# Optimization experiments

Measured on AMD Instinct MI355X. Metric: run time of the kernel, lower is better.

The kernel has to match this reference:

```python
import jax, jax.numpy as jnp
import numpy as np

D_MODEL = 1024
N_HEAD = 16
D_HEAD = D_MODEL // N_HEAD
D_FF = 4096
B, S = 2, 2048
EPS = 1e-5


def setup_inputs() -> dict:
    key = jax.random.key(0)
    ks = jax.random.split(key, 16)
    sc = 1.0 / np.sqrt(D_MODEL)
    x = jax.random.normal(ks[0], (B, S, D_MODEL), dtype=jnp.float32)
    # causal mask: 1 where attention is disallowed (upper triangle)
    mask = jnp.triu(jnp.ones((S, S), dtype=jnp.int32), k=1)[None, None]
    p = {
        'x': x,
        'mask': mask,
        'wq': jax.random.normal(ks[1], (D_MODEL, D_MODEL), jnp.float32) * sc,
        'bq': jnp.zeros((D_MODEL,), jnp.float32),
        'wk': jax.random.normal(ks[2], (D_MODEL, D_MODEL), jnp.float32) * sc,
        'bk': jnp.zeros((D_MODEL,), jnp.float32),
        'wv': jax.random.normal(ks[3], (D_MODEL, D_MODEL), jnp.float32) * sc,
        'bv': jnp.zeros((D_MODEL,), jnp.float32),
        'wo': jax.random.normal(ks[4], (D_MODEL, D_MODEL), jnp.float32) * sc,
        'bo': jnp.zeros((D_MODEL,), jnp.float32),
        'w1': jax.random.normal(ks[5], (D_MODEL, D_FF), jnp.float32) * sc,
        'b1': jnp.zeros((D_FF,), jnp.float32),
        'w2': jax.random.normal(ks[6], (D_FF, D_MODEL), jnp.float32) * (1.0 / np.sqrt(D_FF)),
        'b2': jnp.zeros((D_MODEL,), jnp.float32),
        'g1': jnp.ones((D_MODEL,), jnp.float32),
        'beta1': jnp.zeros((D_MODEL,), jnp.float32),
        'g2': jnp.ones((D_MODEL,), jnp.float32),
        'beta2': jnp.zeros((D_MODEL,), jnp.float32),
    }
    return p


def _layer_norm(x, g, b):
    mu = jnp.mean(x, axis=-1, keepdims=True)
    var = jnp.mean(jnp.square(x - mu), axis=-1, keepdims=True)
    return (x - mu) * jax.lax.rsqrt(var + EPS) * g + b


def reference(x, mask, wq, bq, wk, bk, wv, bv, wo, bo, w1, b1, w2, b2, g1, beta1, g2, beta2):
    b, s, _ = x.shape
    # QKV projections -> [B, H, S, Dh]
    q = (x @ wq + bq).reshape(b, s, N_HEAD, D_HEAD).transpose(0, 2, 1, 3)
    k = (x @ wk + bk).reshape(b, s, N_HEAD, D_HEAD).transpose(0, 2, 1, 3)
    v = (x @ wv + bv).reshape(b, s, N_HEAD, D_HEAD).transpose(0, 2, 1, 3)
    scores = jnp.einsum('bhqd,bhkd->bhqk', q, k) / np.sqrt(D_HEAD)  # [B,H,S,S]
    scores = jnp.where(mask == 1, -jnp.inf, scores)
    attn = jax.nn.softmax(scores, axis=-1)
    out = jnp.einsum('bhqk,bhkd->bhqd', attn, v)
    out = out.transpose(0, 2, 1, 3).reshape(b, s, D_MODEL)
    attn_out = out @ wo + bo
    x1 = _layer_norm(x + attn_out, g1, beta1)
    ffn = jax.nn.relu(x1 @ w1 + b1) @ w2 + b2
    return _layer_norm(x1 + ffn, g2, beta2)
```

## Files before the change

kernel.cpp:

```cpp
#include <hip/hip_runtime.h>
#include <hip/hip_bf16.h>
#include <cstdint>

#define D_MODEL 1024
#define D_FF    4096
#define NHEAD   16
#define DHEAD   64
#define BATCH   2
#define SEQ     2048
#define BT      (BATCH*SEQ)
#define QKVLD   (3*D_MODEL)
#define LN_EPS  1e-5f

typedef __bf16 bf16_t;
typedef bf16_t bf16x8 __attribute__((ext_vector_type(8)));
typedef float  f32x4  __attribute__((ext_vector_type(4)));

__device__ __forceinline__ unsigned short f2b(float f){
  bf16_t h = (bf16_t)f;
  return __builtin_bit_cast(unsigned short, h);
}
__device__ __forceinline__ float b2f(unsigned short u){
  return __builtin_bit_cast(float, ((unsigned int)u)<<16);
}

__device__ __forceinline__ void gload16(const void* g, void* l){
  __builtin_amdgcn_global_load_lds(
      (const __attribute__((address_space(1))) unsigned int*)g,
      (__attribute__((address_space(3))) unsigned int*)l, 16, 0, 0);
}

__global__ __launch_bounds__(256) void cvt_f32_bf16(
    const float* __restrict__ in, unsigned short* __restrict__ out, int n){
  int i = (blockIdx.x*256 + threadIdx.x)*4;
  if (i < n){
    float4 v = *(const float4*)(in + i);
    ushort4 u; u.x=f2b(v.x); u.y=f2b(v.y); u.z=f2b(v.z); u.w=f2b(v.w);
    *(ushort4*)(out + i) = u;
  }
}

__global__ __launch_bounds__(256) void concat_bias(
    const float* __restrict__ bq, const float* __restrict__ bk,
    const float* __restrict__ bv, float* __restrict__ o){
  int i = blockIdx.x*256 + threadIdx.x;
  if (i < D_MODEL){ o[i]=bq[i]; o[D_MODEL+i]=bk[i]; o[2*D_MODEL+i]=bv[i]; }
}

__global__ __launch_bounds__(256) void transpose_cvt(
    const float* __restrict__ in, unsigned short* __restrict__ out, int R, int C){
  __shared__ float t[32][33];
  int c0 = blockIdx.x*32, r0 = blockIdx.y*32;
  int tx = threadIdx.x, ty = threadIdx.y;
  #pragma unroll
  for (int i=0;i<4;++i){ int r = ty + i*8; t[r][tx] = in[(size_t)(r0+r)*C + c0+tx]; }
  __syncthreads();
  #pragma unroll
  for (int i=0;i<4;++i){ int r = ty + i*8; out[(size_t)(c0+r)*R + r0+tx] = f2b(t[tx][r]); }
}

__global__ __launch_bounds__(256) void transpose_cvt4(
    const float* __restrict__ s0, const float* __restrict__ s1,
    const float* __restrict__ s2, const float* __restrict__ s3,
    unsigned short* __restrict__ d0, unsigned short* __restrict__ d1,
    unsigned short* __restrict__ d2, unsigned short* __restrict__ d3){
  __shared__ float t[32][33];
  int z = blockIdx.z;
  const float* in = (z==0)?s0:(z==1)?s1:(z==2)?s2:s3;
  unsigned short* out = (z==0)?d0:(z==1)?d1:(z==2)?d2:d3;
  int c0 = blockIdx.x*32, r0 = blockIdx.y*32;
  int tx = threadIdx.x, ty = threadIdx.y;
  #pragma unroll
  for (int i=0;i<4;++i){ int r = ty + i*8; t[r][tx] = in[(size_t)(r0+r)*D_MODEL + c0+tx]; }
  __syncthreads();
  #pragma unroll
  for (int i=0;i<4;++i){ int r = ty + i*8; out[(size_t)(c0+r)*D_MODEL + r0+tx] = f2b(t[tx][r]); }
}

template<int EPI>
__global__ __launch_bounds__(512,4) void gemm128(
    const unsigned short* __restrict__ A, const unsigned short* __restrict__ Bt,
    const float* __restrict__ bias, const float* __restrict__ resid,
    float* __restrict__ outF, unsigned short* __restrict__ outB,
    int M, int N, int K){
  __shared__ __attribute__((aligned(16))) unsigned short As[2][128*64];
  __shared__ __attribute__((aligned(16))) unsigned short Bs[2][128*64];
  int tid = threadIdx.x;
  int lane = tid & 63, wave = tid >> 6;
  int lr = lane & 15, lg = lane >> 4;
  int row0 = blockIdx.x*128, col0 = blockIdx.y*128;
  int wr = (wave>>2)*64, wc = (wave&3)*32;
  int x7 = lr & 7;

  int sr = tid >> 3;
  int sl = (tid & 7) ^ (sr & 7);
  auto STAGE = [&](int k0, int buf){
    #pragma unroll
    for (int it=0; it<2; ++it){
      int c = it*512 + tid;
      int r = it*64 + sr;
      gload16(A  + (size_t)(row0+r)*K + k0 + sl*8, &As[buf][c<<3]);
      gload16(Bt + (size_t)(col0+r)*K + k0 + sl*8, &Bs[buf][c<<3]);
    }
  };

  f32x4 acc[4][2] = {};
  int nk = K >> 6;
  int t0 = 0, t1 = nk;
  if (EPI==3){ int half = nk >> 1; t0 = blockIdx.z*half; t1 = t0 + half; }
  STAGE(t0<<6, 0);
  asm volatile("s_waitcnt vmcnt(0)" ::: "memory");
  __builtin_amdgcn_s_barrier();
  int cur = 0;
  for (int t=t0; t<t1; ++t){
    if (t+1 < t1) STAGE((t+1)<<6, cur^1);
    #pragma unroll
    for (int kk=0; kk<2; ++kk){
      int sk = ((kk*4 + lg) ^ x7) << 3;
      bf16x8 af[4], bfr[2];
      #pragma unroll
      for (int mi=0;mi<4;++mi) af[mi]  = *(const bf16x8*)&As[cur][(wr+mi*16+lr)*64 + sk];
      #pragma unroll
      for (int ni=0;ni<2;++ni) bfr[ni] = *(const bf16x8*)&Bs[cur][(wc+ni*16+lr)*64 + sk];
      #pragma unroll
      for (int mi=0;mi<4;++mi)
        #pragma unroll
        for (int ni=0;ni<2;++ni)
          acc[mi][ni] = __builtin_amdgcn_mfma_f32_16x16x32_bf16(af[mi], bfr[ni], acc[mi][ni], 0,0,0);
    }
    asm volatile("s_waitcnt vmcnt(0)" ::: "memory");
    __builtin_amdgcn_s_barrier();
    cur ^= 1;
  }
  unsigned short* outBP = (EPI==3) ? (outB + (size_t)blockIdx.z*((size_t)M*N)) : outB;
  #pragma unroll
  for (int mi=0;mi<4;++mi){
    int row = row0 + wr + mi*16 + (lg<<2);
    #pragma unroll
    for (int ni=0;ni<2;++ni){
      int col = col0 + wc + ni*16 + lr;
      float bs = (EPI==3) ? 0.f : bias[col];
      #pragma unroll
      for (int j=0;j<4;++j){
        size_t idx = (size_t)(row+j)*N + col;
        float v = acc[mi][ni][j] + bs;
        if (EPI==3){ outBP[idx] = f2b(v); }
        else if (EPI==2){ v = fmaxf(v, 0.f); outB[idx] = f2b(v); }
        else { outB[idx] = f2b(v); }
      }
    }
  }
}

template<int EPI>
__global__ __launch_bounds__(512,2) void gemm256(
    const unsigned short* __restrict__ A, const unsigned short* __restrict__ Bt,
    const float* __restrict__ bias, unsigned short* __restrict__ outB,
    unsigned short* __restrict__ outVt,
    int M, int N, int K){
  __shared__ __attribute__((aligned(16))) unsigned short As[2][2][128*64];
  __shared__ __attribute__((aligned(16))) unsigned short Bs[2][2][128*64];
  int tid = threadIdx.x;
  int lane = tid & 63, wave = tid >> 6;
  int lr = lane & 15, lg = lane >> 4;
  int wm = wave >> 2, wn = wave & 3;
  int row0 = blockIdx.x*256, col0 = blockIdx.y*256;
  int x7 = lr & 7;
  int sr = tid >> 3;
  int sl = (tid & 7) ^ (sr & 7);

  auto STAGE_A = [&](int t, int buf, int h){
    #pragma unroll
    for (int i=0;i<2;++i){
      int c = i*512 + tid;
      int r = i*64 + sr;
      gload16(A + (size_t)(row0 + h*128 + r)*K + t*64 + sl*8, &As[buf][h][c<<3]);
    }
  };
  auto STAGE_B = [&](int t, int buf, int h){
    #pragma unroll
    for (int i=0;i<2;++i){
      int c = i*512 + tid;
      int r = i*64 + sr;
      gload16(Bt + (size_t)(col0 + h*128 + r)*K + t*64 + sl*8, &Bs[buf][h][c<<3]);
    }
  };

  f32x4 acc[8][4] = {};
  int nk = K >> 6;
  STAGE_B(0,0,0); STAGE_B(0,0,1); STAGE_A(0,0,0); STAGE_A(0,0,1);
  asm volatile("s_waitcnt vmcnt(0)" ::: "memory");
  __builtin_amdgcn_s_barrier();
  int cur = 0;
  int bq = (wn&1)*64;
  for (int t=0; t<nk; ++t){
    bool pre = (t+1 < nk);
    const unsigned short* Ah = &As[cur][wm][0];
    const unsigned short* Bh = &Bs[cur][wn>>1][0];
    bf16x8 af[4][2], bfr[4][2];
    #pragma unroll
    for (int mi=0;mi<4;++mi)
      #pragma unroll
      for (int kk=0;kk<2;++kk)
        af[mi][kk] = *(const bf16x8*)&Ah[(mi*16+lr)*64 + (((kk*4+lg)^x7)<<3)];
    #pragma unroll
    for (int ni=0;ni<2;++ni)
      #pragma unroll
      for (int kk=0;kk<2;++kk)
        bfr[ni][kk] = *(const bf16x8*)&Bh[(bq+ni*16+lr)*64 + (((kk*4+lg)^x7)<<3)];
    if (pre){ STAGE_B(t+1, cur^1, 0);
              asm volatile("s_waitcnt vmcnt(2)" ::: "memory"); }
    else    { asm volatile("s_waitcnt vmcnt(0)" ::: "memory"); }
    __builtin_amdgcn_s_barrier();
    __builtin_amdgcn_s_setprio(1);
    #pragma unroll
    for (int mi=0;mi<4;++mi)
      #pragma unroll
      for (int ni=0;ni<2;++ni)
        #pragma unroll
        for (int kk=0;kk<2;++kk)
          acc[mi][ni] = __builtin_amdgcn_mfma_f32_16x16x32_bf16(af[mi][kk], bfr[ni][kk], acc[mi][ni], 0,0,0);
    __builtin_amdgcn_s_setprio(0);
    __builtin_amdgcn_s_barrier();
    #pragma unroll
    for (int ni=2;ni<4;++ni)
      #pragma unroll
      for (int kk=0;kk<2;++kk)
        bfr[ni][kk] = *(const bf16x8*)&Bh[(bq+ni*16+lr)*64 + (((kk*4+lg)^x7)<<3)];
    if (pre) STAGE_B(t+1, cur^1, 1);
    __builtin_amdgcn_s_barrier();
    __builtin_amdgcn_s_setprio(1);
    #pragma unroll
    for (int mi=0;mi<4;++mi)
      #pragma unroll
      for (int ni=2;ni<4;++ni)
        #pragma unroll
        for (int kk=0;kk<2;++kk)
          acc[mi][ni] = __builtin_amdgcn_mfma_f32_16x16x32_bf16(af[mi][kk], bfr[ni][kk], acc[mi][ni], 0,0,0);
    __builtin_amdgcn_s_setprio(0);
    __builtin_amdgcn_s_barrier();
    #pragma unroll
    for (int mi=0;mi<4;++mi)
      #pragma unroll
      for (int kk=0;kk<2;++kk)
        af[mi][kk] = *(const bf16x8*)&Ah[((mi+4)*16+lr)*64 + (((kk*4+lg)^x7)<<3)];
    if (pre) STAGE_A(t+1, cur^1, 0);
    __builtin_amdgcn_s_barrier();
    __builtin_amdgcn_s_setprio(1);
    #pragma unroll
    for (int mi=0;mi<4;++mi)
      #pragma unroll
      for (int ni=0;ni<2;++ni)
        #pragma unroll
        for (int kk=0;kk<2;++kk)
          acc[mi+4][ni] = __builtin_amdgcn_mfma_f32_16x16x32_bf16(af[mi][kk], bfr[ni][kk], acc[mi+4][ni], 0,0,0);
    __builtin_amdgcn_s_setprio(0);
    __builtin_amdgcn_s_barrier();
    if (pre) STAGE_A(t+1, cur^1, 1);
    __builtin_amdgcn_s_barrier();
    __builtin_amdgcn_s_setprio(1);
    #pragma unroll
    for (int mi=0;mi<4;++mi)
      #pragma unroll
      for (int ni=2;ni<4;++ni)
        #pragma unroll
        for (int kk=0;kk<2;++kk)
          acc[mi+4][ni] = __builtin_amdgcn_mfma_f32_16x16x32_bf16(af[mi][kk], bfr[ni][kk], acc[mi+4][ni], 0,0,0);
    __builtin_amdgcn_s_setprio(0);
    __builtin_amdgcn_s_barrier();
    cur ^= 1;
  }
  #pragma unroll
  for (int mi=0;mi<8;++mi){
    int row = row0 + wm*128 + mi*16 + (lg<<2);
    #pragma unroll
    for (int ni=0;ni<4;++ni){
      int col = col0 + wn*64 + ni*16 + lr;
      float bs = bias[col];
      ushort4 uu;
      #pragma unroll
      for (int j=0;j<4;++j){
        size_t idx = (size_t)(row+j)*N + col;
        float v = acc[mi][ni][j] + bs;
        if (EPI==2) v = fmaxf(v, 0.f);
        unsigned short us = f2b(v);
        outB[idx] = us;
        if (j==0) uu.x=us; else if (j==1) uu.y=us; else if (j==2) uu.z=us; else uu.w=us;
      }
      if (EPI==0 && outVt && col >= 2*D_MODEL){
        int vc = col - 2*D_MODEL;
        int bh = (row>>11)*NHEAD + (vc>>6);
        int d  = vc & 63;
        int s  = row & (SEQ-1);
        *(ushort4*)&outVt[((size_t)bh*DHEAD + d)*SEQ + s] = uu;
      }
    }
  }
}

__global__ __launch_bounds__(256,2) void attn_k(
    const unsigned short* __restrict__ QKV,
    const unsigned short* __restrict__ Vt, unsigned short* __restrict__ O){
  __shared__ __attribute__((aligned(16))) unsigned short Ks[2][128*64];
  __shared__ __attribute__((aligned(16))) unsigned short Vs[2][64*128];
  __shared__ __attribute__((aligned(16))) unsigned short Ps[4][16*128];
  int tid = threadIdx.x, lane = tid&63, wave = tid>>6;
  int lr = lane&15, lg = lane>>4;
  int bid = blockIdx.x;
  int L = (bid & 7)*64 + (bid >> 3);
  int qx = L & 15;
  int bh = L >> 4;
  int b = bh>>4, h = bh&15;
  const int NT = SEQ/64;
  const float SC2 = 0.18033688011112042f;

  #pragma unroll 1
  for (int half=0; half<2; ++half){
    int qt = half ? qx : (NT-1 - qx);
    int q0w = qt*64 + wave*16;

    const unsigned short* Qrow = QKV + (size_t)(b*SEQ + q0w + lr)*QKVLD + h*DHEAD;
    bf16x8 qf[2];
    qf[0] = *(const bf16x8*)(Qrow + lg*8);
    qf[1] = *(const bf16x8*)(Qrow + 32 + lg*8);

    f32x4 oacc[4] = {};
    float m2 = -1e30f, lsum = 0.f;

    auto STAGE = [&](int t, int buf){
      int kv0 = t*128;
      #pragma unroll
      for (int it=0; it<4; ++it){
        int c = it*256 + tid;
        int rk = c>>3, slk = (c&7) ^ (rk&7);
        gload16(QKV + (size_t)(b*SEQ + kv0 + rk)*QKVLD + D_MODEL + h*DHEAD + slk*8, &Ks[buf][c<<3]);
        int rv = c>>4, slv = (c&15) ^ (rv&15);
        gload16(Vt + ((size_t)bh*DHEAD + rv)*SEQ + kv0 + slv*8, &Vs[buf][c<<3]);
      }
    };

    int nkv = (qt + 2) >> 1;
    STAGE(0, 0);
    asm volatile("s_waitcnt vmcnt(0)" ::: "memory");
    __builtin_amdgcn_s_barrier();
    int cur = 0;
    for (int t=0; t<nkv; ++t){
      if (t+1 < nkv) STAGE(t+1, cur^1);

      int kv0 = t*128;
      f32x4 sacc[8] = {};
      #pragma unroll
      for (int kk=0;kk<2;++kk){
        #pragma unroll
        for (int ni=0;ni<8;++ni){
          int krow = ni*16 + lr;
          bf16x8 kf = *(const bf16x8*)&Ks[cur][krow*64 + (((kk*4+lg) ^ (krow&7))<<3)];
          sacc[ni] = __builtin_amdgcn_mfma_f32_16x16x32_bf16(kf, qf[kk], sacc[ni], 0,0,0);
        }
      }
      if (t == nkv-1){
        int qpos = q0w + lr;
        #pragma unroll
        for (int ni=0;ni<8;++ni){
          f32x4 v = sacc[ni];
          #pragma unroll
          for (int j=0;j<4;++j){
            int kpos = kv0 + ni*16 + lg*4 + j;
            float sv = v[j]*SC2;
            v[j] = (kpos > qpos) ? -1e30f : sv;
          }
          sacc[ni] = v;
        }
      } else {
        #pragma unroll
        for (int ni=0;ni<8;++ni) sacc[ni] *= SC2;
      }
      f32x4 vm = sacc[0];
      #pragma unroll
      for (int ni=1;ni<8;++ni)
        #pragma unroll
        for (int j=0;j<4;++j) vm[j] = fmaxf(vm[j], sacc[ni][j]);
      float rm = fmaxf(fmaxf(vm[0],vm[1]), fmaxf(vm[2],vm[3]));
      rm = fmaxf(rm, __shfl_xor(rm, 16));
      rm = fmaxf(rm, __shfl_xor(rm, 32));
      if (__all(rm <= m2)){
        f32x4 vs = {};
        #pragma unroll
        for (int ni=0;ni<8;++ni){
          f32x4 p;
          #pragma unroll
          for (int j=0;j<4;++j){ p[j] = exp2f(sacc[ni][j] - m2); vs[j] += p[j]; }
          sacc[ni] = p;
        }
        float rs = (vs[0]+vs[1]) + (vs[2]+vs[3]);
        rs += __shfl_xor(rs, 16);
        rs += __shfl_xor(rs, 32);
        lsum += rs;
      } else {
        float mnew = fmaxf(m2, rm);
        float corr = exp2f(m2 - mnew);
        m2 = mnew;
        f32x4 vs = {};
        #pragma unroll
        for (int ni=0;ni<8;++ni){
          f32x4 p;
          #pragma unroll
          for (int j=0;j<4;++j){ p[j] = exp2f(sacc[ni][j] - mnew); vs[j] += p[j]; }
          sacc[ni] = p;
        }
        float rs = (vs[0]+vs[1]) + (vs[2]+vs[3]);
        rs += __shfl_xor(rs, 16);
        rs += __shfl_xor(rs, 32);
        lsum = lsum*corr + rs;
        #pragma unroll
        for (int j=0;j<4;++j){
          float cj = __shfl(corr, lg*4 + j);
          #pragma unroll
          for (int nd=0; nd<4; ++nd) oacc[nd][j] *= cj;
        }
      }
      #pragma unroll
      for (int ni=0;ni<8;++ni){
        ushort4 u; u.x=f2b(sacc[ni][0]); u.y=f2b(sacc[ni][1]);
                   u.z=f2b(sacc[ni][2]); u.w=f2b(sacc[ni][3]);
        int ts = ni*2 + (lg>>1);
        int a = lr*128 + (((ts ^ lr))<<3) + ((lg&1)<<2);
        *(uint2*)&Ps[wave][a] = __builtin_bit_cast(uint2, u);
      }
      #pragma unroll
      for (int kk=0;kk<4;++kk){
        bf16x8 pa = *(const bf16x8*)&Ps[wave][lr*128 + (((kk*4+lg) ^ lr)<<3)];
        #pragma unroll
        for (int nd=0; nd<4; ++nd){
          int dr = nd*16 + lr;
          bf16x8 vf = *(const bf16x8*)&Vs[cur][dr*128 + (((kk*4+lg) ^ (dr&15))<<3)];
          oacc[nd] = __builtin_amdgcn_mfma_f32_16x16x32_bf16(pa, vf, oacc[nd], 0,0,0);
        }
      }
      asm volatile("s_waitcnt vmcnt(0)" ::: "memory");
      __builtin_amdgcn_s_barrier();
      cur ^= 1;
    }
    #pragma unroll
    for (int j=0;j<4;++j){
      float lj = __shfl(lsum, lg*4 + j);
      float inv = 1.f / lj;
      int token = b*SEQ + q0w + lg*4 + j;
      #pragma unroll
      for (int nd=0; nd<4; ++nd)
        O[(size_t)token*D_MODEL + h*DHEAD + nd*16 + lr] = f2b(oacc[nd][j]*inv);
    }
  }
}

template<int MODE>
__global__ __launch_bounds__(256) void ln_sum_k(
    const unsigned short* __restrict__ P,
    const float* __restrict__ bias,
    const float* __restrict__ resid,
    const float* __restrict__ g, const float* __restrict__ bta,
    float* __restrict__ outF, unsigned short* __restrict__ outB){
  int row = blockIdx.x, tid = threadIdx.x;
  const size_t MN = (size_t)BT*D_MODEL;
  ushort4 a0 = ((const ushort4*)(P + (size_t)row*D_MODEL))[tid];
  ushort4 a1 = ((const ushort4*)(P + MN + (size_t)row*D_MODEL))[tid];
  float4 rr = ((const float4*)(resid + (size_t)row*D_MODEL))[tid];
  float4 bb = ((const float4*)bias)[tid];
  float4 v;
  v.x = b2f(a0.x)+b2f(a1.x)+bb.x+rr.x; v.y = b2f(a0.y)+b2f(a1.y)+bb.y+rr.y;
  v.z = b2f(a0.z)+b2f(a1.z)+bb.z+rr.z; v.w = b2f(a0.w)+b2f(a1.w)+bb.w+rr.w;
  float s = v.x+v.y+v.z+v.w;
  float q = v.x*v.x+v.y*v.y+v.z*v.z+v.w*v.w;
  #pragma unroll
  for (int d=32; d; d>>=1){ s += __shfl_xor(s, d); q += __shfl_xor(q, d); }
  __shared__ float rs[4], rq[4];
  int wave = tid>>6;
  if ((tid&63)==0){ rs[wave]=s; rq[wave]=q; }
  __syncthreads();
  s = rs[0]+rs[1]+rs[2]+rs[3];
  q = rq[0]+rq[1]+rq[2]+rq[3];
  float mu  = s * (1.f/D_MODEL);
  float var = q * (1.f/D_MODEL) - mu*mu;
  float rstd = rsqrtf(var + LN_EPS);
  float4 gg = ((const float4*)g)[tid];
  float4 be = ((const float4*)bta)[tid];
  float o0 = (v.x-mu)*rstd*gg.x + be.x;
  float o1 = (v.y-mu)*rstd*gg.y + be.y;
  float o2 = (v.z-mu)*rstd*gg.z + be.z;
  float o3 = (v.w-mu)*rstd*gg.w + be.w;
  float4 o; o.x=o0; o.y=o1; o.z=o2; o.w=o3;
  ((float4*)(outF + (size_t)row*D_MODEL))[tid] = o;
  if (MODE==0){
    ushort4 u; u.x=f2b(o0); u.y=f2b(o1); u.z=f2b(o2); u.w=f2b(o3);
    ((ushort4*)(outB + (size_t)row*D_MODEL))[tid] = u;
  }
}

extern "C" void kernel_launch(void* const* d_in, const int* in_sizes, int n_in,
                              void* d_out, int out_size, void* d_ws, size_t ws_size,
                              hipStream_t stream){
  const float* x  = (const float*)d_in[0];
  const float* wq = (const float*)d_in[2];  const float* bq = (const float*)d_in[3];
  const float* wk = (const float*)d_in[4];  const float* bk = (const float*)d_in[5];
  const float* wv = (const float*)d_in[6];  const float* bv = (const float*)d_in[7];
  const float* wo = (const float*)d_in[8];  const float* bo = (const float*)d_in[9];
  const float* w1 = (const float*)d_in[10]; const float* b1 = (const float*)d_in[11];
  const float* w2 = (const float*)d_in[12]; const float* b2 = (const float*)d_in[13];
  const float* g1 = (const float*)d_in[14]; const float* be1= (const float*)d_in[15];
  const float* g2 = (const float*)d_in[16]; const float* be2= (const float*)d_in[17];

  char* w = (char*)d_ws;
  size_t off = 0;
  auto nxt = [&](size_t bytes)->void*{
    void* p = w + off; off = (off + bytes + 255) & ~(size_t)255; return p;
  };
  unsigned short* xb    = (unsigned short*)nxt((size_t)BT*D_MODEL*2);
  unsigned short* wqkvT = (unsigned short*)nxt((size_t)QKVLD*D_MODEL*2);
  unsigned short* woT   = (unsigned short*)nxt((size_t)D_MODEL*D_MODEL*2);
  unsigned short* w1T   = (unsigned short*)nxt((size_t)D_MODEL*D_FF*2);
  unsigned short* w2T   = (unsigned short*)nxt((size_t)D_MODEL*D_FF*2);
  float*          bqkv  = (float*)nxt((size_t)QKVLD*4);
  unsigned short* QKV   = (unsigned short*)nxt((size_t)BT*QKVLD*2);
  unsigned short* VtG   = (unsigned short*)nxt((size_t)BT*D_MODEL*2);
  unsigned short* attnb = (unsigned short*)nxt((size_t)BT*D_MODEL*2);
  float*          x1f   = (float*)nxt((size_t)BT*D_MODEL*4);
  unsigned short* ffn1  = (unsigned short*)nxt((size_t)BT*D_FF*2);
  unsigned short* Psum  = QKV;
  unsigned short* x1b   = attnb;

  dim3 tb(32,8);
  cvt_f32_bf16<<<(BT*D_MODEL)/1024, 256, 0, stream>>>(x, xb, BT*D_MODEL);
  concat_bias<<<4, 256, 0, stream>>>(bq, bk, bv, bqkv);
  transpose_cvt4<<<dim3(D_MODEL/32, D_MODEL/32, 4), tb, 0, stream>>>(
      wq, wk, wv, wo,
      wqkvT, wqkvT + D_MODEL*D_MODEL, wqkvT + 2*D_MODEL*D_MODEL, woT);
  transpose_cvt<<<dim3(D_FF/32,    D_MODEL/32), tb, 0, stream>>>(w1, w1T, D_MODEL, D_FF);
  transpose_cvt<<<dim3(D_MODEL/32, D_FF/32),    tb, 0, stream>>>(w2, w2T, D_FF, D_MODEL);

  gemm256<0><<<dim3(BT/256, QKVLD/256), 512, 0, stream>>>(xb, wqkvT, bqkv, QKV, VtG, BT, QKVLD, D_MODEL);

  attn_k<<<512, 256, 0, stream>>>(QKV, VtG, attnb);

  gemm128<3><<<dim3(BT/128, D_MODEL/128, 2), 512, 0, stream>>>(attnb, woT, nullptr, nullptr, nullptr, Psum, BT, D_MODEL, D_MODEL);
  ln_sum_k<0><<<BT, 256, 0, stream>>>(Psum, bo, x, g1, be1, x1f, x1b);

  gemm256<2><<<dim3(BT/256, D_FF/256), 512, 0, stream>>>(x1b, w1T, b1, ffn1, nullptr, BT, D_FF, D_MODEL);

  gemm128<3><<<dim3(BT/128, D_MODEL/128, 2), 512, 0, stream>>>(ffn1, w2T, nullptr, nullptr, nullptr, Psum, BT, D_MODEL, D_FF);
  ln_sum_k<1><<<BT, 256, 0, stream>>>(Psum, b2, x1f, g2, be2, (float*)d_out, nullptr);
}
```

Baseline: 222.3 us.

## Software-pipeline attention: overlap next tile QK with current softmax and PV

Restructures the flash-attention inner loop so the QK^T MFMAs for tile t run before the softmax and PV of tile t-1. K and V loads are staged separately: K for t+1 is issued early and V for t+1 only after PV frees its buffer, with a partial vmcnt wait. The goal is to hide softmax latency behind matrix work and overlap global loads more finely. The cost is a second 8-register score array, which may raise register pressure and lower occupancy, plus an extra barrier per iteration.

```diff
diff --git a/kernel.cpp b/kernel.cpp
--- a/kernel.cpp
+++ b/kernel.cpp
@@ -327,59 +327,57 @@
     f32x4 oacc[4] = {};
     float m2 = -1e30f, lsum = 0.f;
 
-    auto STAGE = [&](int t, int buf){
+    auto STAGE_K = [&](int t, int buf){
       int kv0 = t*128;
       #pragma unroll
       for (int it=0; it<4; ++it){
         int c = it*256 + tid;
         int rk = c>>3, slk = (c&7) ^ (rk&7);
         gload16(QKV + (size_t)(b*SEQ + kv0 + rk)*QKVLD + D_MODEL + h*DHEAD + slk*8, &Ks[buf][c<<3]);
+      }
+    };
+    auto STAGE_V = [&](int t, int buf){
+      int kv0 = t*128;
+      #pragma unroll
+      for (int it=0; it<4; ++it){
+        int c = it*256 + tid;
         int rv = c>>4, slv = (c&15) ^ (rv&15);
         gload16(Vt + ((size_t)bh*DHEAD + rv)*SEQ + kv0 + slv*8, &Vs[buf][c<<3]);
       }
     };
-
-    int nkv = (qt + 2) >> 1;
-    STAGE(0, 0);
-    asm volatile("s_waitcnt vmcnt(0)" ::: "memory");
-    __builtin_amdgcn_s_barrier();
-    int cur = 0;
-    for (int t=0; t<nkv; ++t){
-      if (t+1 < nkv) STAGE(t+1, cur^1);
-
-      int kv0 = t*128;
-      f32x4 sacc[8] = {};
-      #pragma unroll
-      for (int kk=0;kk<2;++kk){
+    auto QK = [&](f32x4 (&s)[8], int kb){
+      #pragma unroll
+      for (int kk=0;kk<2;++kk)
         #pragma unroll
         for (int ni=0;ni<8;++ni){
           int krow = ni*16 + lr;
-          bf16x8 kf = *(const bf16x8*)&Ks[cur][krow*64 + (((kk*4+lg) ^ (krow&7))<<3)];
-          sacc[ni] = __builtin_amdgcn_mfma_f32_16x16x32_bf16(kf, qf[kk], sacc[ni], 0,0,0);
+          bf16x8 kf = *(const bf16x8*)&Ks[kb][krow*64 + (((kk*4+lg) ^ (krow&7))<<3)];
+          s[ni] = __builtin_amdgcn_mfma_f32_16x16x32_bf16(kf, qf[kk], s[ni], 0,0,0);
         }
-      }
-      if (t == nkv-1){
+    };
+    auto SOFTMAX = [&](f32x4 (&s)[8], int kv0, bool diag){
+      if (diag){
         int qpos = q0w + lr;
         #pragma unroll
         for (int ni=0;ni<8;++ni){
-          f32x4 v = sacc[ni];
+          f32x4 v = s[ni];
           #pragma unroll
           for (int j=0;j<4;++j){
             int kpos = kv0 + ni*16 + lg*4 + j;
             float sv = v[j]*SC2;
             v[j] = (kpos > qpos) ? -1e30f : sv;
           }
-          sacc[ni] = v;
+          s[ni] = v;
         }
       } else {
         #pragma unroll
-        for (int ni=0;ni<8;++ni) sacc[ni] *= SC2;
-      }
-      f32x4 vm = sacc[0];
+        for (int ni=0;ni<8;++ni) s[ni] *= SC2;
+      }
+      f32x4 vm = s[0];
       #pragma unroll
       for (int ni=1;ni<8;++ni)
         #pragma unroll
-        for (int j=0;j<4;++j) vm[j] = fmaxf(vm[j], sacc[ni][j]);
+        for (int j=0;j<4;++j) vm[j] = fmaxf(vm[j], s[ni][j]);
       float rm = fmaxf(fmaxf(vm[0],vm[1]), fmaxf(vm[2],vm[3]));
       rm = fmaxf(rm, __shfl_xor(rm, 16));
       rm = fmaxf(rm, __shfl_xor(rm, 32));
@@ -389,8 +387,8 @@
         for (int ni=0;ni<8;++ni){
           f32x4 p;
           #pragma unroll
-          for (int j=0;j<4;++j){ p[j] = exp2f(sacc[ni][j] - m2); vs[j] += p[j]; }
-          sacc[ni] = p;
+          for (int j=0;j<4;++j){ p[j] = exp2f(s[ni][j] - m2); vs[j] += p[j]; }
+          s[ni] = p;
         }
         float rs = (vs[0]+vs[1]) + (vs[2]+vs[3]);
         rs += __shfl_xor(rs, 16);
@@ -405,8 +403,8 @@
         for (int ni=0;ni<8;++ni){
           f32x4 p;
           #pragma unroll
-          for (int j=0;j<4;++j){ p[j] = exp2f(sacc[ni][j] - mnew); vs[j] += p[j]; }
-          sacc[ni] = p;
+          for (int j=0;j<4;++j){ p[j] = exp2f(s[ni][j] - mnew); vs[j] += p[j]; }
+          s[ni] = p;
         }
         float rs = (vs[0]+vs[1]) + (vs[2]+vs[3]);
         rs += __shfl_xor(rs, 16);
@@ -421,26 +419,54 @@
       }
       #pragma unroll
       for (int ni=0;ni<8;++ni){
-        ushort4 u; u.x=f2b(sacc[ni][0]); u.y=f2b(sacc[ni][1]);
-                   u.z=f2b(sacc[ni][2]); u.w=f2b(sacc[ni][3]);
+        ushort4 u; u.x=f2b(s[ni][0]); u.y=f2b(s[ni][1]);
+                   u.z=f2b(s[ni][2]); u.w=f2b(s[ni][3]);
         int ts = ni*2 + (lg>>1);
         int a = lr*128 + (((ts ^ lr))<<3) + ((lg&1)<<2);
         *(uint2*)&Ps[wave][a] = __builtin_bit_cast(uint2, u);
       }
+    };
+    auto PV = [&](int vb){
       #pragma unroll
       for (int kk=0;kk<4;++kk){
         bf16x8 pa = *(const bf16x8*)&Ps[wave][lr*128 + (((kk*4+lg) ^ lr)<<3)];
         #pragma unroll
         for (int nd=0; nd<4; ++nd){
           int dr = nd*16 + lr;
-          bf16x8 vf = *(const bf16x8*)&Vs[cur][dr*128 + (((kk*4+lg) ^ (dr&15))<<3)];
+          bf16x8 vf = *(const bf16x8*)&Vs[vb][dr*128 + (((kk*4+lg) ^ (dr&15))<<3)];
           oacc[nd] = __builtin_amdgcn_mfma_f32_16x16x32_bf16(pa, vf, oacc[nd], 0,0,0);
         }
       }
-      asm volatile("s_waitcnt vmcnt(0)" ::: "memory");
+    };
+
+    int nkv = (qt + 2) >> 1;
+    __builtin_amdgcn_s_barrier();
+    STAGE_K(0,0); STAGE_V(0,0);
+    if (nkv > 1){ STAGE_K(1,1); STAGE_V(1,1); }
+    asm volatile("s_waitcnt vmcnt(0)" ::: "memory");
+    __builtin_amdgcn_s_barrier();
+    f32x4 sN[8] = {};
+    QK(sN, 0);
+    #pragma unroll 1
+    for (int t=1; t<nkv; ++t){
+      if (t+1 < nkv) STAGE_K(t+1, (t+1)&1);
+      f32x4 sT[8] = {};
+      QK(sT, t&1);
+      SOFTMAX(sN, (t-1)*128, false);
+      PV((t-1)&1);
       __builtin_amdgcn_s_barrier();
-      cur ^= 1;
-    }
+      if (t+1 < nkv){
+        STAGE_V(t+1, (t+1)&1);
+        asm volatile("s_waitcnt vmcnt(4)" ::: "memory");
+      } else {
+        asm volatile("s_waitcnt vmcnt(0)" ::: "memory");
+      }
+      __builtin_amdgcn_s_barrier();
+      #pragma unroll
+      for (int i=0;i<8;++i) sN[i] = sT[i];
+    }
+    SOFTMAX(sN, (nkv-1)*128, true);
+    PV((nkv-1)&1);
     #pragma unroll
     for (int j=0;j<4;++j){
       float lj = __shfl(lsum, lg*4 + j);
```

Result: no change. 226.5 us (+1.9%).
